# Optimization experiments

Hardware: AMD Instinct MI355X
Metric: run time of the kernel (lower is better)

The kernel has to match this reference:

```python
import jax, jax.numpy as jnp
import numpy as np

D = 768
H = 12
DH = 64
S = 1500
SCALE = 0.125  # 1/sqrt(64)


def setup_inputs() -> dict:
    key = jax.random.key(0)
    ks = jax.random.split(key, 8)
    def w(k):
        return jax.random.normal(k, (D, D), dtype=jnp.float32) * (1.0 / np.sqrt(D))
    x = jax.random.normal(ks[0], (8, S, D), dtype=jnp.float32)
    return {
        "x": x,
        "Wq": w(ks[1]), "bq": jax.random.normal(ks[2], (D,), dtype=jnp.float32) * 0.02,
        "Wk": w(ks[3]),
        "Wv": w(ks[4]), "bv": jax.random.normal(ks[5], (D,), dtype=jnp.float32) * 0.02,
        "Wo": w(ks[6]), "bo": jax.random.normal(ks[7], (D,), dtype=jnp.float32) * 0.02,
    }


def reference(x, Wq, bq, Wk, Wv, bv, Wo, bo):
    B = x.shape[0]
    # torch Linear: y = x @ W.T + b
    q = (jnp.einsum('bsd,ed->bse', x, Wq) + bq) * SCALE
    k = jnp.einsum('bsd,ed->bse', x, Wk)
    v = jnp.einsum('bsd,ed->bse', x, Wv) + bv
    # split heads: [B, S, H, DH] -> [B, H, S, DH]
    q = q.reshape(B, S, H, DH).transpose(0, 2, 1, 3)
    k = k.reshape(B, S, H, DH).transpose(0, 2, 1, 3)
    v = v.reshape(B, S, H, DH).transpose(0, 2, 1, 3)
    scores = jnp.einsum('bhqd,bhkd->bhqk', q, k)  # [B, H, S, S]
    probs = jax.nn.softmax(scores, axis=-1)
    ctx = jnp.einsum('bhqk,bhkd->bhqd', probs, v)
    ctx = ctx.transpose(0, 2, 1, 3).reshape(B, S, D)
    return jnp.einsum('bsd,ed->bse', ctx, Wo) + bo
```

## Files before the change

kernel.cpp:

```cpp
#include <hip/hip_runtime.h>
#include <hip/hip_bf16.h>

constexpr int kD  = 768;
constexpr int kH  = 12;
constexpr int kDH = 64;
constexpr int kS  = 1500;
constexpr int kSP = 1504;
constexpr int kB  = 8;
constexpr int kM  = kB * kS;
constexpr float kScale = 0.125f;
constexpr int kPSTR = 72;

typedef __bf16 bf16;
typedef __bf16 bf16x4 __attribute__((ext_vector_type(4)));
typedef __bf16 bf16x8 __attribute__((ext_vector_type(8)));
typedef float  floatx4 __attribute__((ext_vector_type(4)));

__global__ __launch_bounds__(256) void detect_kernel(const void* __restrict__ xraw,
                                                     int* __restrict__ flag) {
    __shared__ int bad;
    if (threadIdx.x == 0) bad = 0;
    __syncthreads();
    const bf16* xb = (const bf16*)xraw;
    int c = 0;
    for (int k = 0; k < 16; k++) {
        int idx = 2 * (threadIdx.x + 256 * k);
        float v = fabsf((float)xb[idx]);
        if (!(v == 0.0f || (v > 1e-20f && v < 1e6f))) c++;
    }
    atomicAdd(&bad, c);
    __syncthreads();
    if (threadIdx.x == 0) *flag = (bad > 8) ? 1 : 0;
}

__global__ __launch_bounds__(256) void cvt_bf16_kernel(const void* __restrict__ src,
                                                       bf16* __restrict__ dst, int n,
                                                       const int* __restrict__ flag) {
    int i = blockIdx.x * 256 + threadIdx.x;
    if (i < n) {
        if (*flag)
            dst[i] = (bf16)((const float*)src)[i];
        else
            dst[i] = ((const bf16*)src)[i];
    }
}

__global__ __launch_bounds__(256) void cvt_f32_kernel(const void* __restrict__ src,
                                                      float* __restrict__ dst, int n,
                                                      const int* __restrict__ flag) {
    int i = blockIdx.x * 256 + threadIdx.x;
    if (i < n) {
        if (*flag)
            dst[i] = ((const float*)src)[i];
        else
            dst[i] = (float)((const bf16*)src)[i];
    }
}

__global__ __launch_bounds__(256) void zeropad_kernel(bf16* __restrict__ q_ws,
                                                      bf16* __restrict__ k_ws,
                                                      bf16* __restrict__ vt_ws) {
    int t = blockIdx.x * 256 + threadIdx.x;
    if (t < kB * kH * (kSP - kS) * kDH) {
        int bh  = t >> 8;
        int rem = t & 255;
        int s   = kS + (rem >> 6);
        int dh  = rem & 63;
        size_t qi = ((size_t)bh * kSP + s) * kDH + dh;
        q_ws[qi] = (bf16)0.f;
        k_ws[qi] = (bf16)0.f;
        size_t vi = ((size_t)bh * kDH + dh) * kSP + s;
        vt_ws[vi] = (bf16)0.f;
    }
}

__device__ __forceinline__ void async_copy16(const bf16* g, bf16* l) {
    __builtin_amdgcn_global_load_lds(
        (const __attribute__((address_space(1))) void*)g,
        (__attribute__((address_space(3))) void*)l,
        16, 0, 0);
}

__device__ __forceinline__ void gemm128_db(const bf16* __restrict__ X,
                                           const bf16* __restrict__ W,
                                           int m0, int n0,
                                           bf16* Asm, bf16* Bsm,
                                           floatx4 acc[4][4]) {
    const int tid  = threadIdx.x;
    const int lane = tid & 63;
    const int w    = tid >> 6;
    const int srow = (w << 4) + (lane >> 2);
    const int scol = (lane & 3) << 3;
    const int lrow = lane & 15;
    const int lq   = lane >> 4;
    const int wm   = (w >> 1) << 6;
    const int wn   = (w & 1) << 6;

    const bf16* gA = X + (size_t)(m0 + srow) * kD + scol;
    const bf16* gB = W + (size_t)(n0 + srow) * kD + scol;
    const int wof = w << 9;

    async_copy16(gA, Asm + wof);
    async_copy16(gA + (size_t)64 * kD, Asm + wof + 2048);
    async_copy16(gB, Bsm + wof);
    async_copy16(gB + (size_t)64 * kD, Bsm + wof + 2048);
    asm volatile("s_waitcnt vmcnt(0)" ::: "memory");
    __builtin_amdgcn_s_barrier();

    for (int ks = 0; ks < kD / 32; ks++) {
        const int cur = ks & 1;
        if (ks + 1 < kD / 32) {
            const int nb = (cur ^ 1) << 12;
            const int k0 = (ks + 1) * 32;
            async_copy16(gA + k0, Asm + nb + wof);
            async_copy16(gA + (size_t)64 * kD + k0, Asm + nb + wof + 2048);
            async_copy16(gB + k0, Bsm + nb + wof);
            async_copy16(gB + (size_t)64 * kD + k0, Bsm + nb + wof + 2048);
        }
        const bf16* A = Asm + (cur << 12);
        const bf16* B = Bsm + (cur << 12);
        bf16x8 af[4], bfr[4];
#pragma unroll
        for (int i = 0; i < 4; i++)
            af[i] = *(const bf16x8*)(A + ((wm + i * 16 + lrow) << 5) + (lq << 3));
#pragma unroll
        for (int j = 0; j < 4; j++)
            bfr[j] = *(const bf16x8*)(B + ((wn + j * 16 + lrow) << 5) + (lq << 3));
#pragma unroll
        for (int i = 0; i < 4; i++)
#pragma unroll
            for (int j = 0; j < 4; j++)
                acc[i][j] = __builtin_amdgcn_mfma_f32_16x16x32_bf16(
                    af[i], bfr[j], acc[i][j], 0, 0, 0);
        asm volatile("s_waitcnt vmcnt(0)" ::: "memory");
        __builtin_amdgcn_s_barrier();
    }
}

__global__ __launch_bounds__(256) void qkv_kernel(const bf16* __restrict__ X,
                                                  const bf16* __restrict__ Wq,
                                                  const bf16* __restrict__ Wk,
                                                  const bf16* __restrict__ Wv,
                                                  const float* __restrict__ bq,
                                                  const float* __restrict__ bv,
                                                  bf16* __restrict__ q_ws,
                                                  bf16* __restrict__ k_ws,
                                                  bf16* __restrict__ vt_ws) {
    __shared__ bf16 Asm[2 * 4096];
    __shared__ bf16 Bsm[2 * 4096];

    const int lin = blockIdx.x;
    const int wk  = (lin & 7) * 212 + (lin >> 3);
    if (wk >= 94 * 18) return;
    const int bx  = wk / 18;
    const int r   = wk - bx * 18;
    const int m0  = bx << 7;
    const int mat = r / 6;
    const int n0  = (r % 6) << 7;
    const bf16* W = (mat == 0) ? Wq : (mat == 1) ? Wk : Wv;

    floatx4 acc[4][4] = {};
    gemm128_db(X, W, m0, n0, Asm, Bsm, acc);

    const int tid  = threadIdx.x;
    const int lane = tid & 63;
    const int w    = tid >> 6;
    const int lrow = lane & 15;
    const int lq   = lane >> 4;
    const int wm   = (w >> 1) << 6;
    const int wn   = (w & 1) << 6;

#pragma unroll
    for (int i = 0; i < 4; i++) {
#pragma unroll
        for (int j = 0; j < 4; j++) {
            const int n  = n0 + wn + j * 16 + lrow;
            const int hh = n >> 6, dh = n & 63;
            const float bval = (mat == 0) ? bq[n] : (mat == 2) ? bv[n] : 0.f;
#pragma unroll
            for (int r2 = 0; r2 < 4; r2++) {
                const int m = m0 + wm + i * 16 + lq * 4 + r2;
                if (m >= kM) continue;
                float v = acc[i][j][r2];
                if (mat == 0)      v = (v + bval) * kScale;
                else if (mat == 2) v = v + bval;
                const int bb = m / kS, s = m - bb * kS;
                if (mat == 2)
                    vt_ws[(((size_t)(bb * kH + hh)) * kDH + dh) * kSP + s] = (bf16)v;
                else if (mat == 1)
                    k_ws[(((size_t)(bb * kH + hh)) * kSP + s) * kDH + dh] = (bf16)v;
                else
                    q_ws[(((size_t)(bb * kH + hh)) * kSP + s) * kDH + dh] = (bf16)v;
            }
        }
    }
}

__global__ __launch_bounds__(256) void out_kernel(const bf16* __restrict__ X,
                                                  const bf16* __restrict__ Wo,
                                                  const float* __restrict__ bo,
                                                  float* __restrict__ outf) {
    __shared__ bf16 Asm[2 * 4096];
    __shared__ bf16 Bsm[2 * 4096];

    const int m0 = blockIdx.x << 7;
    const int n0 = blockIdx.y << 7;

    floatx4 acc[4][4] = {};
    gemm128_db(X, Wo, m0, n0, Asm, Bsm, acc);

    const int tid  = threadIdx.x;
    const int lane = tid & 63;
    const int w    = tid >> 6;
    const int lrow = lane & 15;
    const int lq   = lane >> 4;
    const int wm   = (w >> 1) << 6;
    const int wn   = (w & 1) << 6;

#pragma unroll
    for (int i = 0; i < 4; i++) {
#pragma unroll
        for (int j = 0; j < 4; j++) {
            const int n = n0 + wn + j * 16 + lrow;
            const float bval = bo[n];
#pragma unroll
            for (int r = 0; r < 4; r++) {
                const int m = m0 + wm + i * 16 + lq * 4 + r;
                if (m >= kM) continue;
                outf[(size_t)m * kD + n] = acc[i][j][r] + bval;
            }
        }
    }
}

__device__ __forceinline__ const bf16* lds_at(const bf16* sm, int row, int cb) {
    return sm + row * 64 + ((cb ^ ((row & 7) << 4)) >> 1);
}

__device__ __forceinline__ void stage_k(const bf16* __restrict__ kbase, int s0,
                                        bf16* ksm, int w, int lane) {
#pragma unroll
    for (int i = 0; i < 2; i++) {
        const int sidx = i * 4 + w;
        const int row  = sidx * 8 + (lane >> 3);
        const int cb   = (lane & 7) << 4;
        const int scb  = cb ^ ((row & 7) << 4);
        int gr = s0 + row;
        if (gr >= kSP) gr = 1472;
        async_copy16(kbase + (size_t)gr * kDH + (scb >> 1), ksm + sidx * 512);
    }
}

__device__ __forceinline__ void stage_v(const bf16* __restrict__ vbase, int s0,
                                        bf16* vsm, int w, int lane) {
#pragma unroll
    for (int i = 0; i < 2; i++) {
        const int sidx = i * 4 + w;
        const int row  = sidx * 8 + (lane >> 3);
        const int cb   = (lane & 7) << 4;
        const int scb  = cb ^ ((row & 7) << 4);
        int key = s0 + (scb >> 1);
        if (key >= kSP) key = 1472;
        async_copy16(vbase + (size_t)row * kSP + key, vsm + sidx * 512);
    }
}

__device__ __forceinline__ void qk_mfma_lds(const bf16* ksm,
                                            const bf16x8 qf[2][2],
                                            floatx4 sc[2][4],
                                            int col, int quad) {
#pragma unroll
    for (int t = 0; t < 4; t++) {
        const int r = 16 * t + col;
        const bf16x8 kf0 = *(const bf16x8*)lds_at(ksm, r, quad * 16);
        const bf16x8 kf1 = *(const bf16x8*)lds_at(ksm, r, 64 + quad * 16);
        __builtin_amdgcn_s_setprio(1);
#pragma unroll
        for (int qt = 0; qt < 2; qt++) {
            floatx4 a = {0.f, 0.f, 0.f, 0.f};
            a = __builtin_amdgcn_mfma_f32_16x16x32_bf16(kf0, qf[qt][0], a, 0, 0, 0);
            a = __builtin_amdgcn_mfma_f32_16x16x32_bf16(kf1, qf[qt][1], a, 0, 0, 0);
            sc[qt][t] = a;
        }
        __builtin_amdgcn_s_setprio(0);
    }
}

template <bool MASK>
__device__ __forceinline__ void exp_store(const floatx4 sc[2][4],
                                          bf16* __restrict__ Pw,
                                          float lsum[2],
                                          int s0, int col, int quad) {
#pragma unroll
    for (int qt = 0; qt < 2; qt++)
#pragma unroll
        for (int t = 0; t < 4; t++) {
            bf16x4 pv;
#pragma unroll
            for (int r = 0; r < 4; r++) {
                float p;
                if (MASK && (s0 + 16 * t + quad * 4 + r >= kS))
                    p = 0.f;
                else
                    p = __expf(sc[qt][t][r]);
                lsum[qt] += p;
                pv[r] = (bf16)p;
            }
            *(bf16x4*)(Pw + (qt * 16 + col) * kPSTR + 16 * t + quad * 4) = pv;
        }
}

__device__ __forceinline__ void pv_lds(const bf16* vsm,
                                       const bf16* __restrict__ Pr,
                                       floatx4 Oacc[2][4],
                                       int col, int quad) {
    bf16x8 pa[2][2];
#pragma unroll
    for (int qt = 0; qt < 2; qt++)
#pragma unroll
        for (int kc = 0; kc < 2; kc++)
            pa[qt][kc] = *(const bf16x8*)(Pr + (qt * 16 + col) * kPSTR + kc * 32 + quad * 8);
#pragma unroll
    for (int n = 0; n < 4; n++) {
        const int row = n * 16 + col;
#pragma unroll
        for (int kc = 0; kc < 2; kc++) {
            const bf16x8 vf = *(const bf16x8*)lds_at(vsm, row, kc * 64 + quad * 16);
            __builtin_amdgcn_s_setprio(1);
#pragma unroll
            for (int qt = 0; qt < 2; qt++)
                Oacc[qt][n] = __builtin_amdgcn_mfma_f32_16x16x32_bf16(
                    pa[qt][kc], vf, Oacc[qt][n], 0, 0, 0);
            __builtin_amdgcn_s_setprio(0);
        }
    }
}

__global__ __launch_bounds__(256, 2) void fattn_kernel(const bf16* __restrict__ q_ws,
                                                       const bf16* __restrict__ k_ws,
                                                       const bf16* __restrict__ vt_ws,
                                                       bf16* __restrict__ ctx) {
    __shared__ bf16 Ksm[2][64 * 64];
    __shared__ bf16 Vsm[2][64 * 64];
    __shared__ bf16 Pbuf[4][32 * kPSTR];

    const int idx = blockIdx.x;
    const int bh  = idx % 96;
    const int qb  = idx / 96;
    const int b   = bh / kH;
    const int h   = bh - b * kH;
    const int tid  = threadIdx.x;
    const int w    = tid >> 6;
    const int lane = tid & 63;
    const int col  = lane & 15;
    const int quad = lane >> 4;
    const int q0   = qb * 128 + w * 32;
    const bool active = (q0 < kS);

    const bf16* qbase = q_ws  + (size_t)bh * kSP * kDH;
    const bf16* kbase = k_ws  + (size_t)bh * kSP * kDH;
    const bf16* vbase = vt_ws + (size_t)bh * kDH * kSP;

    bf16x8 qf[2][2] = {};
    if (active) {
#pragma unroll
        for (int qt = 0; qt < 2; qt++) {
            const bf16* qr = qbase + (size_t)(q0 + qt * 16 + col) * kDH + quad * 8;
            qf[qt][0] = *(const bf16x8*)(qr);
            qf[qt][1] = *(const bf16x8*)(qr + 32);
        }
    }

    float lsum[2] = {0.f, 0.f};
    floatx4 Oacc[2][4];
#pragma unroll
    for (int qt = 0; qt < 2; qt++)
#pragma unroll
        for (int n = 0; n < 4; n++) Oacc[qt][n] = (floatx4){0.f, 0.f, 0.f, 0.f};

    bf16* const P = &Pbuf[w][0];
    floatx4 sc[2][4];

    stage_k(kbase, 0, &Ksm[0][0], w, lane);
    stage_v(vbase, 0, &Vsm[0][0], w, lane);
    __syncthreads();

    int buf = 0;
    for (int c = 0; c < 23; ++c) {
        stage_k(kbase, (c + 1) * 64, &Ksm[buf ^ 1][0], w, lane);
        stage_v(vbase, (c + 1) * 64, &Vsm[buf ^ 1][0], w, lane);
        if (active) {
            qk_mfma_lds(&Ksm[buf][0], qf, sc, col, quad);
            exp_store<false>(sc, P, lsum, c * 64, col, quad);
            pv_lds(&Vsm[buf][0], P, Oacc, col, quad);
        }
        __syncthreads();
        buf ^= 1;
    }
    if (active) {
        qk_mfma_lds(&Ksm[buf][0], qf, sc, col, quad);
        exp_store<true>(sc, P, lsum, 1472, col, quad);
        pv_lds(&Vsm[buf][0], P, Oacc, col, quad);

#pragma unroll
        for (int qt = 0; qt < 2; qt++) {
            float l = lsum[qt];
            l += __shfl_xor(l, 16);
            l += __shfl_xor(l, 32);
            const float rinv_col = 1.0f / l;
            float ri[4];
#pragma unroll
            for (int r = 0; r < 4; r++)
                ri[r] = __shfl(rinv_col, quad * 4 + r, 16);
#pragma unroll
            for (int n = 0; n < 4; n++)
#pragma unroll
                for (int r = 0; r < 4; r++) {
                    const int q = q0 + qt * 16 + quad * 4 + r;
                    if (q < kS)
                        ctx[((size_t)(b * kS + q)) * kD + h * kDH + n * 16 + col] =
                            (bf16)(Oacc[qt][n][r] * ri[r]);
                }
        }
    }
}

extern "C" void kernel_launch(void* const* d_in, const int* in_sizes, int n_in,
                              void* d_out, int out_size, void* d_ws, size_t ws_size,
                              hipStream_t stream) {
    float* out_f = (float*)d_out;

    constexpr size_t nX = (size_t)kM * kD;
    constexpr size_t nW = (size_t)kD * kD;
    constexpr size_t per_qkv = (size_t)kB * kH * kSP * kDH;

    bf16* xb    = (bf16*)d_ws;
    bf16* Wqb   = xb + nX;
    bf16* Wkb   = Wqb + nW;
    bf16* Wvb   = Wkb + nW;
    bf16* Wob   = Wvb + nW;
    bf16* q_ws  = Wob + nW;
    bf16* k_ws  = q_ws + per_qkv;
    bf16* vt_ws = k_ws + per_qkv;
    float* bqf  = (float*)(vt_ws + per_qkv);
    float* bvf  = bqf + kD;
    float* bof  = bvf + kD;
    int*  flag  = (int*)(bof + kD);
    bf16* ctx   = xb;

    detect_kernel<<<1, 256, 0, stream>>>(d_in[0], flag);
    cvt_bf16_kernel<<<(int)((nX + 255) / 256), 256, 0, stream>>>(d_in[0], xb,  (int)nX, flag);
    cvt_bf16_kernel<<<(int)((nW + 255) / 256), 256, 0, stream>>>(d_in[1], Wqb, (int)nW, flag);
    cvt_bf16_kernel<<<(int)((nW + 255) / 256), 256, 0, stream>>>(d_in[3], Wkb, (int)nW, flag);
    cvt_bf16_kernel<<<(int)((nW + 255) / 256), 256, 0, stream>>>(d_in[4], Wvb, (int)nW, flag);
    cvt_bf16_kernel<<<(int)((nW + 255) / 256), 256, 0, stream>>>(d_in[6], Wob, (int)nW, flag);
    cvt_f32_kernel<<<3, 256, 0, stream>>>(d_in[2], bqf, kD, flag);
    cvt_f32_kernel<<<3, 256, 0, stream>>>(d_in[5], bvf, kD, flag);
    cvt_f32_kernel<<<3, 256, 0, stream>>>(d_in[7], bof, kD, flag);

    zeropad_kernel<<<96, 256, 0, stream>>>(q_ws, k_ws, vt_ws);
    qkv_kernel<<<dim3(1696), 256, 0, stream>>>(xb, Wqb, Wkb, Wvb, bqf, bvf,
                                               q_ws, k_ws, vt_ws);

    fattn_kernel<<<dim3(12 * 96), 256, 0, stream>>>(q_ws, k_ws, vt_ws, ctx);

    dim3 ogrid((kM + 127) / 128, kD / 128);
    out_kernel<<<ogrid, 256, 0, stream>>>(ctx, Wob, bof, out_f);
}
```

Measured before the change: 356.3 us.

## Triple-buffer GEMM LDS pipeline with partial vmcnt waits

Replaces the double-buffered K loop in the QKV and output projection GEMMs with a three-stage LDS ring. Loads are issued two K-steps ahead and the wait uses vmcnt(4), so one stage's loads can stay in flight across the barrier. The goal is to hide global-load latency that the full vmcnt(0) wait used to expose each step. It raises LDS per block from 32KB to 48KB, which may reduce occupancy, and it fully unrolls the K loop.

```diff
diff --git a/kernel.cpp b/kernel.cpp
--- a/kernel.cpp
+++ b/kernel.cpp
@@ -10,6 +10,7 @@
 constexpr int kM  = kB * kS;
 constexpr float kScale = 0.125f;
 constexpr int kPSTR = 72;
+constexpr int kNK = kD / 32;
 
 typedef __bf16 bf16;
 typedef __bf16 bf16x4 __attribute__((ext_vector_type(4)));
@@ -81,7 +82,46 @@
         16, 0, 0);
 }
 
-__device__ __forceinline__ void gemm128_db(const bf16* __restrict__ X,
+#define G_STAGE(KK, SB)                                                         \
+    {                                                                           \
+        const int k0_ = (KK) * 32;                                              \
+        async_copy16(gA + k0_, Asm + (SB) * 4096 + wof);                        \
+        async_copy16(gA + (size_t)64 * kD + k0_, Asm + (SB) * 4096 + wof + 2048); \
+        async_copy16(gB + k0_, Bsm + (SB) * 4096 + wof);                        \
+        async_copy16(gB + (size_t)64 * kD + k0_, Bsm + (SB) * 4096 + wof + 2048); \
+    }
+
+#define G_COMPUTE(CB)                                                           \
+    {                                                                           \
+        const bf16* A_ = Asm + (CB) * 4096;                                     \
+        const bf16* B_ = Bsm + (CB) * 4096;                                     \
+        bf16x8 af[4], bfr[4];                                                   \
+        _Pragma("unroll") for (int i = 0; i < 4; i++)                           \
+            af[i] = *(const bf16x8*)(A_ + ((wm + i * 16 + lrow) << 5) + (lq << 3)); \
+        _Pragma("unroll") for (int j = 0; j < 4; j++)                           \
+            bfr[j] = *(const bf16x8*)(B_ + ((wn + j * 16 + lrow) << 5) + (lq << 3)); \
+        _Pragma("unroll") for (int i = 0; i < 4; i++)                           \
+            _Pragma("unroll") for (int j = 0; j < 4; j++)                       \
+                acc[i][j] = __builtin_amdgcn_mfma_f32_16x16x32_bf16(            \
+                    af[i], bfr[j], acc[i][j], 0, 0, 0);                         \
+    }
+
+#define G_STEP(KK, CB, SB)                                                      \
+    {                                                                           \
+        if ((KK) + 2 < kNK) G_STAGE((KK) + 2, SB);                              \
+        G_COMPUTE(CB);                                                          \
+        if ((KK) + 1 < kNK) {                                                   \
+            if ((KK) + 2 < kNK) {                                               \
+                asm volatile("s_waitcnt vmcnt(4)" ::: "memory");                \
+            } else {                                                            \
+                asm volatile("s_waitcnt vmcnt(0)" ::: "memory");                \
+            }                                                                   \
+            __builtin_amdgcn_s_barrier();                                       \
+            __builtin_amdgcn_sched_barrier(0);                                  \
+        }                                                                       \
+    }
+
+__device__ __forceinline__ void gemm128_tb(const bf16* __restrict__ X,
                                            const bf16* __restrict__ W,
                                            int m0, int n0,
                                            bf16* Asm, bf16* Bsm,
@@ -100,40 +140,17 @@
     const bf16* gB = W + (size_t)(n0 + srow) * kD + scol;
     const int wof = w << 9;
 
-    async_copy16(gA, Asm + wof);
-    async_copy16(gA + (size_t)64 * kD, Asm + wof + 2048);
-    async_copy16(gB, Bsm + wof);
-    async_copy16(gB + (size_t)64 * kD, Bsm + wof + 2048);
-    asm volatile("s_waitcnt vmcnt(0)" ::: "memory");
+    G_STAGE(0, 0);
+    G_STAGE(1, 1);
+    asm volatile("s_waitcnt vmcnt(4)" ::: "memory");
     __builtin_amdgcn_s_barrier();
-
-    for (int ks = 0; ks < kD / 32; ks++) {
-        const int cur = ks & 1;
-        if (ks + 1 < kD / 32) {
-            const int nb = (cur ^ 1) << 12;
-            const int k0 = (ks + 1) * 32;
-            async_copy16(gA + k0, Asm + nb + wof);
-            async_copy16(gA + (size_t)64 * kD + k0, Asm + nb + wof + 2048);
-            async_copy16(gB + k0, Bsm + nb + wof);
-            async_copy16(gB + (size_t)64 * kD + k0, Bsm + nb + wof + 2048);
-        }
-        const bf16* A = Asm + (cur << 12);
-        const bf16* B = Bsm + (cur << 12);
-        bf16x8 af[4], bfr[4];
-#pragma unroll
-        for (int i = 0; i < 4; i++)
-            af[i] = *(const bf16x8*)(A + ((wm + i * 16 + lrow) << 5) + (lq << 3));
-#pragma unroll
-        for (int j = 0; j < 4; j++)
-            bfr[j] = *(const bf16x8*)(B + ((wn + j * 16 + lrow) << 5) + (lq << 3));
-#pragma unroll
-        for (int i = 0; i < 4; i++)
-#pragma unroll
-            for (int j = 0; j < 4; j++)
-                acc[i][j] = __builtin_amdgcn_mfma_f32_16x16x32_bf16(
-                    af[i], bfr[j], acc[i][j], 0, 0, 0);
-        asm volatile("s_waitcnt vmcnt(0)" ::: "memory");
-        __builtin_amdgcn_s_barrier();
+    __builtin_amdgcn_sched_barrier(0);
+
+#pragma unroll
+    for (int ks = 0; ks < kNK; ks += 3) {
+        G_STEP(ks,     0, 2);
+        G_STEP(ks + 1, 1, 0);
+        G_STEP(ks + 2, 2, 1);
     }
 }
 
@@ -146,8 +163,8 @@
                                                   bf16* __restrict__ q_ws,
                                                   bf16* __restrict__ k_ws,
                                                   bf16* __restrict__ vt_ws) {
-    __shared__ bf16 Asm[2 * 4096];
-    __shared__ bf16 Bsm[2 * 4096];
+    __shared__ bf16 Asm[3 * 4096];
+    __shared__ bf16 Bsm[3 * 4096];
 
     const int lin = blockIdx.x;
     const int wk  = (lin & 7) * 212 + (lin >> 3);
@@ -160,7 +177,7 @@
     const bf16* W = (mat == 0) ? Wq : (mat == 1) ? Wk : Wv;
 
     floatx4 acc[4][4] = {};
-    gemm128_db(X, W, m0, n0, Asm, Bsm, acc);
+    gemm128_tb(X, W, m0, n0, Asm, Bsm, acc);
 
     const int tid  = threadIdx.x;
     const int lane = tid & 63;
@@ -200,14 +217,14 @@
                                                   const bf16* __restrict__ Wo,
                                                   const float* __restrict__ bo,
                                                   float* __restrict__ outf) {
-    __shared__ bf16 Asm[2 * 4096];
-    __shared__ bf16 Bsm[2 * 4096];
+    __shared__ bf16 Asm[3 * 4096];
+    __shared__ bf16 Bsm[3 * 4096];
 
     const int m0 = blockIdx.x << 7;
     const int n0 = blockIdx.y << 7;
 
     floatx4 acc[4][4] = {};
-    gemm128_db(X, Wo, m0, n0, Asm, Bsm, acc);
+    gemm128_tb(X, Wo, m0, n0, Asm, Bsm, acc);
 
     const int tid  = threadIdx.x;
     const int lane = tid & 63;
```

Result: faster. 344.7 us, median of 2 (-3.3%).
